# Optimization experiments

Hardware: AMD Instinct MI355X
Metric: run time of the kernel (lower is better)

The kernel has to match this reference:

```python
import jax, jax.numpy as jnp
import numpy as np

N_USERS = 60000
N_ITEMS = 40000
N = N_USERS + N_ITEMS   # ncount
EMB = 64
NNZ = 3200000           # nnz of sparse_norm_adj (avg degree 32)
LN_EPS = 1e-5


def setup_inputs() -> dict:
    key = jax.random.key(0)
    ks = jax.random.split(key, 12)
    ego = jax.random.normal(ks[0], (N, EMB), jnp.float32) * 0.1
    rows = jax.random.randint(ks[1], (NNZ,), 0, N)
    cols = jax.random.randint(ks[2], (NNZ,), 0, N)
    # normalized adjacency values (non-trainable buffer)
    vals = jax.random.uniform(ks[3], (NNZ,), jnp.float32) * 0.01
    # xavier-uniform-ish scale for [64,64]: sqrt(2/(64+64)) = 0.125
    w_uu = jax.random.normal(ks[4], (EMB, EMB), jnp.float32) * 0.125
    filt_uu = jax.random.uniform(ks[5], (N_USERS,), jnp.float32, 0.99, 1.01)
    par_uu = jax.random.uniform(ks[6], (2,), jnp.float32, 0.0, 0.99)
    w_ii = jax.random.normal(ks[7], (EMB, EMB), jnp.float32) * 0.125
    filt_ii = jax.random.uniform(ks[8], (N_ITEMS,), jnp.float32, 0.99, 1.01)
    par_ii = jax.random.uniform(ks[9], (2,), jnp.float32, 0.0, 0.99)
    ln_gamma = jnp.ones((EMB,), jnp.float32)
    ln_beta = jnp.zeros((EMB,), jnp.float32)
    return {"ego_embeddings": ego, "rows": rows, "cols": cols, "vals": vals,
            "w_uu": w_uu, "filt_uu": filt_uu, "par_uu": par_uu,
            "w_ii": w_ii, "filt_ii": filt_ii, "par_ii": par_ii,
            "ln_gamma": ln_gamma, "ln_beta": ln_beta}


def _spmm(rows, cols, vals, x):
    # out[rows] += vals * x[cols]  <=>  sparse_adj @ x
    return jax.ops.segment_sum(vals[:, None] * x[cols], rows, num_segments=N)


def reference(ego_embeddings, rows, cols, vals, w_uu, filt_uu, par_uu,
              w_ii, filt_ii, par_ii, ln_gamma, ln_beta):
    res = ego_embeddings
    u = ego_embeddings[:N_USERS]
    it = ego_embeddings[N_USERS:]
    # HWNN layer with K1=K2=1 collapses to par0*par1 * diag(filter) @ X @ W
    user_ego = par_uu[0] * par_uu[1] * ((filt_uu[:, None] * u) @ w_uu) + u
    item_ego = par_ii[0] * par_ii[1] * ((filt_ii[:, None] * it) @ w_ii) + it
    ego = jnp.concatenate([user_ego, item_ego], axis=0)  # [N, EMB]
    # HGCNConv (act=False): adj @ (adj.T @ ego)
    h = jax.ops.segment_sum(vals[:, None] * ego[rows], cols, num_segments=N)  # adj.T @ ego
    y = _spmm(rows, cols, vals, h)                                            # adj @ h
    # LayerNorm (eps=1e-5, affine) + residual from the ORIGINAL input
    mu = jnp.mean(y, axis=-1, keepdims=True)
    var = jnp.var(y, axis=-1, keepdims=True)
    yn = (y - mu) / jnp.sqrt(var + LN_EPS) * ln_gamma + ln_beta
    out = yn + res
    return out[:N_USERS], out[N_USERS:]
```

## Files before the change

kernel.cpp:

```cpp
#include <hip/hip_runtime.h>

#define N_USERS 60000
#define N_ITEMS 40000
#define N_TOTAL 100000
#define EMB 64
#define LN_EPS 1e-5f

#define KPS 512
#define KSH 9
#define NSUP ((N_TOTAL + KPS - 1) / KPS)
#define EPB 4096
#define TR_ROWS 32
#define XPITCH 68
#define CAP 3584

__device__ __forceinline__ float bf2f(unsigned short h)
{ return __uint_as_float(((unsigned)h) << 16); }
__device__ __forceinline__ unsigned short f2bf(float f)
{
    unsigned u = __float_as_uint(f);
    return (unsigned short)((u + 0x7FFFu + ((u >> 16) & 1u)) >> 16);
}

__global__ void transform_tile(const float* __restrict__ x,
                               const float* __restrict__ w_uu,
                               const float* __restrict__ filt_uu,
                               const float* __restrict__ par_uu,
                               const float* __restrict__ w_ii,
                               const float* __restrict__ filt_ii,
                               const float* __restrict__ par_ii,
                               unsigned short* __restrict__ out)
{
    __shared__ float Wls[EMB * EMB];
    __shared__ float xs[TR_ROWS * XPITCH];
    const int tid = threadIdx.x;
    const int r0 = blockIdx.x * TR_ROWS;
    const int itm = (r0 >= N_USERS);
    const float* W  = itm ? w_ii : w_uu;
    const float* fb = itm ? filt_ii : filt_uu;
    const int foff  = itm ? N_USERS : 0;
    const float c   = itm ? par_ii[0] * par_ii[1] : par_uu[0] * par_uu[1];

    for (int i = tid; i < EMB * EMB / 4; i += 256)
        ((float4*)Wls)[i] = ((const float4*)W)[i];
    for (int i = tid; i < TR_ROWS * 16; i += 256) {
        const float4 v = ((const float4*)x)[r0 * 16 + i];
        *(float4*)&xs[(i >> 4) * XPITCH + (i & 15) * 4] = v;
    }
    __syncthreads();

    const int lane = tid & 63;
    const int wv = tid >> 6;
    const int rg = lane >> 4;
    const int j  = lane & 15;

#pragma unroll
    for (int it = 0; it < 2; ++it) {
        const int rl = wv * 8 + it * 4 + rg;
        const int row = r0 + rl;
        float4 acc = make_float4(0.f, 0.f, 0.f, 0.f);
#pragma unroll 8
        for (int k = 0; k < EMB; ++k) {
            const float xb = xs[rl * XPITCH + k];
            const float4 w4 = *(const float4*)&Wls[k * EMB + 4 * j];
            acc.x += xb * w4.x; acc.y += xb * w4.y;
            acc.z += xb * w4.z; acc.w += xb * w4.w;
        }
        const float cf = c * fb[row - foff];
        const float4 xv = *(const float4*)&xs[rl * XPITCH + 4 * j];
        ushort4 o;
        o.x = f2bf(cf * acc.x + xv.x);
        o.y = f2bf(cf * acc.y + xv.y);
        o.z = f2bf(cf * acc.z + xv.z);
        o.w = f2bf(cf * acc.w + xv.w);
        *(ushort4*)&out[(size_t)row * EMB + 4 * j] = o;
    }
}

__global__ void hist_sup(const int* __restrict__ rows,
                         const int* __restrict__ cols,
                         int* __restrict__ cnt_r,
                         int* __restrict__ cnt_c, int nnz)
{
    __shared__ int hr[NSUP], hc[NSUP];
    const int tid = threadIdx.x;
    for (int i = tid; i < NSUP; i += 256) { hr[i] = 0; hc[i] = 0; }
    __syncthreads();
    for (int e = blockIdx.x * 256 + tid; e < nnz; e += gridDim.x * 256) {
        atomicAdd(&hr[rows[e] >> KSH], 1);
        atomicAdd(&hc[cols[e] >> KSH], 1);
    }
    __syncthreads();
    for (int i = tid; i < NSUP; i += 256) {
        if (hr[i]) atomicAdd(&cnt_r[i], hr[i]);
        if (hc[i]) atomicAdd(&cnt_c[i], hc[i]);
    }
}

__global__ void scan_sup(const int* __restrict__ cnt_c, int* __restrict__ base_c,
                         int* __restrict__ cur_c,
                         const int* __restrict__ cnt_r, int* __restrict__ base_r,
                         int* __restrict__ cur_r)
{
    const int* cnt = blockIdx.x ? cnt_r : cnt_c;
    int* base = blockIdx.x ? base_r : base_c;
    int* cur  = blockIdx.x ? cur_r  : cur_c;
    __shared__ int wsum[4];
    const int lane = threadIdx.x & 63;
    const int wv = threadIdx.x >> 6;
    const int i = threadIdx.x;
    const int v = (i < NSUP) ? cnt[i] : 0;
    int incl = v;
#pragma unroll
    for (int off = 1; off < 64; off <<= 1) {
        const int t = __shfl_up(incl, off, 64);
        if (lane >= off) incl += t;
    }
    if (lane == 63) wsum[wv] = incl;
    __syncthreads();
    int woff = 0;
    for (int w = 0; w < wv; ++w) woff += wsum[w];
    const int excl = woff + incl - v;
    if (i < NSUP) { base[i] = excl; cur[i] = excl; }
    if (i == 0) base[NSUP] = wsum[0] + wsum[1] + wsum[2] + wsum[3];
}

__global__ void __launch_bounds__(256, 1)
build_l1(const int* __restrict__ key,
         const int* __restrict__ other,
         const float* __restrict__ vals,
         int* __restrict__ cursor,
         int2* __restrict__ pairs1, int nnz)
{
    __shared__ int2 stage[EPB];
    __shared__ unsigned char sg[EPB];
    __shared__ int hist[NSUP];
    __shared__ int sexcl[NSUP];
    __shared__ int gbase[NSUP];
    __shared__ int lcur[NSUP];
    __shared__ int wsum[4];

    const int tid = threadIdx.x;
    const int e0 = blockIdx.x * EPB;
    const int ecnt = min(EPB, nnz - e0);

    for (int i = tid; i < NSUP; i += 256) hist[i] = 0;
    __syncthreads();

    int myk[16], myo[16];
    float myv[16];
#pragma unroll
    for (int i = 0; i < 16; ++i) {
        const int s = tid + i * 256;
        if (s < ecnt) {
            const int e = e0 + s;
            myk[i] = key[e]; myo[i] = other[e]; myv[i] = vals[e];
            atomicAdd(&hist[myk[i] >> KSH], 1);
        } else myk[i] = -1;
    }
    __syncthreads();

    {
        const int lane = tid & 63;
        const int wv = tid >> 6;
        const int v = (tid < NSUP) ? hist[tid] : 0;
        int incl = v;
#pragma unroll
        for (int off = 1; off < 64; off <<= 1) {
            const int t = __shfl_up(incl, off, 64);
            if (lane >= off) incl += t;
        }
        if (lane == 63) wsum[wv] = incl;
        __syncthreads();
        int woff = 0;
        for (int w = 0; w < wv; ++w) woff += wsum[w];
        const int excl = woff + incl - v;
        if (tid < NSUP) {
            sexcl[tid] = excl;
            lcur[tid] = excl;
            gbase[tid] = v ? atomicAdd(&cursor[tid], v) : 0;
        }
    }
    __syncthreads();

#pragma unroll
    for (int i = 0; i < 16; ++i) {
        if (myk[i] >= 0) {
            const int g = myk[i] >> KSH;
            const int s = atomicAdd(&lcur[g], 1);
            stage[s] = make_int2(myo[i] | ((myk[i] & (KPS - 1)) << 20),
                                 __float_as_int(myv[i]));
            sg[s] = (unsigned char)g;
        }
    }
    __syncthreads();

    for (int s = tid; s < ecnt; s += 256) {
        const int g = sg[s];
        pairs1[gbase[g] + (s - sexcl[g])] = stage[s];
    }
}

template <bool LN>
__global__ void __launch_bounds__(1024, 1)
spmm_fused(const int* __restrict__ base,
           const int2* __restrict__ pairs,
           const unsigned short* __restrict__ src,
           const float* __restrict__ ego,
           const float* __restrict__ gamma,
           const float* __restrict__ beta,
           unsigned short* __restrict__ dstb,
           float* __restrict__ dstf)
{
    __shared__ int2 stage[CAP];
    __shared__ int2 sorted[CAP];
    __shared__ int cnt[KPS];
    __shared__ int kbase[KPS];
    __shared__ int kcur[KPS];

    const int tid = threadIdx.x;
    const int sup = blockIdx.x;
    const int beg = base[sup];
    const int end = base[sup + 1];
    const int g = tid >> 4;
    const int l = tid & 15;

    float4 acc[8];
#pragma unroll
    for (int i = 0; i < 8; ++i) acc[i] = make_float4(0.f, 0.f, 0.f, 0.f);

    if (tid < KPS) cnt[tid] = 0;
    __syncthreads();

    int c0 = beg;
    int csz = min(CAP, end - c0);
    for (int i = tid; i < csz; i += 1024) {
        const int2 v = pairs[c0 + i];
        stage[i] = v;
        atomicAdd(&cnt[(v.x >> 20) & (KPS - 1)], 1);
    }
    __syncthreads();

    while (csz > 0) {
        if (tid < 64) {
            int c[8]; int tsum = 0;
#pragma unroll
            for (int u = 0; u < 8; ++u) { c[u] = cnt[tid * 8 + u]; tsum += c[u]; }
            int incl = tsum;
#pragma unroll
            for (int off = 1; off < 64; off <<= 1) {
                const int t = __shfl_up(incl, off, 64);
                if (tid >= off) incl += t;
            }
            int run = incl - tsum;
#pragma unroll
            for (int u = 0; u < 8; ++u) {
                kbase[tid * 8 + u] = run;
                kcur[tid * 8 + u]  = run;
                run += c[u];
                cnt[tid * 8 + u] = 0;
            }
        }
        __syncthreads();

        for (int i = tid; i < csz; i += 1024) {
            const int2 v = stage[i];
            const int pos = atomicAdd(&kcur[(v.x >> 20) & (KPS - 1)], 1);
            sorted[pos] = v;
        }
        __syncthreads();

        const int nc0 = c0 + csz;
        const int ncsz = min(CAP, end - nc0);

#pragma unroll
        for (int rr = 0; rr < 8; ++rr) {
            const int k = g * 8 + rr;
            int j = kbase[k];
            const int e = kcur[k];
            float4 a = acc[rr];
            for (; j + 4 <= e; j += 4) {
                const int2 p0 = sorted[j];
                const int2 p1 = sorted[j + 1];
                const int2 p2 = sorted[j + 2];
                const int2 p3 = sorted[j + 3];
                const ushort4 s0 = ((const ushort4*)(src + (size_t)(p0.x & 0x1FFFF) * EMB))[l];
                const ushort4 s1 = ((const ushort4*)(src + (size_t)(p1.x & 0x1FFFF) * EMB))[l];
                const ushort4 s2 = ((const ushort4*)(src + (size_t)(p2.x & 0x1FFFF) * EMB))[l];
                const ushort4 s3 = ((const ushort4*)(src + (size_t)(p3.x & 0x1FFFF) * EMB))[l];
                const float v0 = __int_as_float(p0.y);
                const float v1 = __int_as_float(p1.y);
                const float v2 = __int_as_float(p2.y);
                const float v3 = __int_as_float(p3.y);
                a.x += v0 * bf2f(s0.x); a.y += v0 * bf2f(s0.y);
                a.z += v0 * bf2f(s0.z); a.w += v0 * bf2f(s0.w);
                a.x += v1 * bf2f(s1.x); a.y += v1 * bf2f(s1.y);
                a.z += v1 * bf2f(s1.z); a.w += v1 * bf2f(s1.w);
                a.x += v2 * bf2f(s2.x); a.y += v2 * bf2f(s2.y);
                a.z += v2 * bf2f(s2.z); a.w += v2 * bf2f(s2.w);
                a.x += v3 * bf2f(s3.x); a.y += v3 * bf2f(s3.y);
                a.z += v3 * bf2f(s3.z); a.w += v3 * bf2f(s3.w);
            }
            for (; j < e; ++j) {
                const int2 p = sorted[j];
                const ushort4 s = ((const ushort4*)(src + (size_t)(p.x & 0x1FFFF) * EMB))[l];
                const float v = __int_as_float(p.y);
                a.x += v * bf2f(s.x); a.y += v * bf2f(s.y);
                a.z += v * bf2f(s.z); a.w += v * bf2f(s.w);
            }
            acc[rr] = a;
        }

        for (int i = tid; i < ncsz; i += 1024) {
            const int2 v = pairs[nc0 + i];
            stage[i] = v;
            atomicAdd(&cnt[(v.x >> 20) & (KPS - 1)], 1);
        }
        c0 = nc0; csz = ncsz;
        __syncthreads();
    }

    const int r0 = sup * KPS + g * 8;
    if (!LN) {
#pragma unroll
        for (int rr = 0; rr < 8; ++rr) {
            const int row = r0 + rr;
            if (row < N_TOTAL) {
                ushort4 o;
                o.x = f2bf(acc[rr].x); o.y = f2bf(acc[rr].y);
                o.z = f2bf(acc[rr].z); o.w = f2bf(acc[rr].w);
                ((ushort4*)dstb)[(size_t)row * 16 + l] = o;
            }
        }
    } else {
        const float4 gm = ((const float4*)gamma)[l];
        const float4 bt = ((const float4*)beta)[l];
#pragma unroll
        for (int rr = 0; rr < 8; ++rr) {
            const int row = r0 + rr;
            const float4 a = acc[rr];
            float s  = a.x + a.y + a.z + a.w;
            float s2 = a.x * a.x + a.y * a.y + a.z * a.z + a.w * a.w;
#pragma unroll
            for (int m = 1; m <= 8; m <<= 1) {
                s  += __shfl_xor(s,  m, 64);
                s2 += __shfl_xor(s2, m, 64);
            }
            const float mu  = s * (1.0f / EMB);
            const float var = s2 * (1.0f / EMB) - mu * mu;
            const float inv = rsqrtf(var + LN_EPS);
            if (row < N_TOTAL) {
                const float4 eg = ((const float4*)(ego + (size_t)row * EMB))[l];
                float4 o;
                o.x = (a.x - mu) * inv * gm.x + bt.x + eg.x;
                o.y = (a.y - mu) * inv * gm.y + bt.y + eg.y;
                o.z = (a.z - mu) * inv * gm.z + bt.z + eg.z;
                o.w = (a.w - mu) * inv * gm.w + bt.w + eg.w;
                ((float4*)(dstf + (size_t)row * EMB))[l] = o;
            }
        }
    }
}

__global__ void transform_kernel(const float* __restrict__ x,
                                 const float* __restrict__ W,
                                 const float* __restrict__ filt,
                                 const float* __restrict__ par,
                                 float* __restrict__ out, int nrows)
{
    __shared__ float Ws[EMB * EMB];
    const int tid = threadIdx.x;
    for (int i = tid; i < EMB * EMB; i += blockDim.x) Ws[i] = W[i];
    __syncthreads();
    const float c = par[0] * par[1];
    const int lane = tid & 63;
    const int wave = tid >> 6;
    const int r0 = blockIdx.x * 32;
    for (int rr = wave; rr < 32; rr += 4) {
        const int r = r0 + rr;
        if (r >= nrows) break;
        const float xv = x[(size_t)r * EMB + lane];
        float acc = 0.f;
#pragma unroll
        for (int k = 0; k < EMB; ++k) {
            const float xk = __shfl(xv, k, 64);
            acc += xk * Ws[k * EMB + lane];
        }
        out[(size_t)r * EMB + lane] = c * filt[r] * acc + xv;
    }
}

__global__ void spmm_scatter(const int* __restrict__ src_idx,
                             const int* __restrict__ dst_idx,
                             const float* __restrict__ vals,
                             const float* __restrict__ src,
                             float* __restrict__ dst, int nnz)
{
    const long long t = (long long)blockIdx.x * blockDim.x + threadIdx.x;
    const int e = (int)(t >> 4);
    const int l = (int)(t & 15);
    if (e >= nnz) return;
    const int s = src_idx[e];
    const int d = dst_idx[e];
    const float v = vals[e];
    const float4 xv = ((const float4*)(src + (size_t)s * EMB))[l];
    float* dp = dst + (size_t)d * EMB + l * 4;
    atomicAdd(dp + 0, v * xv.x);
    atomicAdd(dp + 1, v * xv.y);
    atomicAdd(dp + 2, v * xv.z);
    atomicAdd(dp + 3, v * xv.w);
}

__global__ void ln_residual(const float* y,
                            const float* __restrict__ ego,
                            const float* __restrict__ gamma,
                            const float* __restrict__ beta,
                            float* out, int nrows)
{
    const int lane = threadIdx.x & 63;
    const int wave = threadIdx.x >> 6;
    const int r = blockIdx.x * 4 + wave;
    if (r >= nrows) return;
    const float v = y[(size_t)r * EMB + lane];
    float s = v, s2 = v * v;
#pragma unroll
    for (int off = 32; off > 0; off >>= 1) {
        s  += __shfl_down(s,  off, 64);
        s2 += __shfl_down(s2, off, 64);
    }
    s  = __shfl(s,  0, 64);
    s2 = __shfl(s2, 0, 64);
    const float mu  = s * (1.0f / EMB);
    const float var = s2 * (1.0f / EMB) - mu * mu;
    const float inv = rsqrtf(var + LN_EPS);
    out[(size_t)r * EMB + lane] =
        (v - mu) * inv * gamma[lane] + beta[lane] + ego[(size_t)r * EMB + lane];
}

extern "C" void kernel_launch(void* const* d_in, const int* in_sizes, int n_in,
                              void* d_out, int out_size, void* d_ws, size_t ws_size,
                              hipStream_t stream)
{
    const float* ego     = (const float*)d_in[0];
    const int*   rows    = (const int*)  d_in[1];
    const int*   cols    = (const int*)  d_in[2];
    const float* vals    = (const float*)d_in[3];
    const float* w_uu    = (const float*)d_in[4];
    const float* filt_uu = (const float*)d_in[5];
    const float* par_uu  = (const float*)d_in[6];
    const float* w_ii    = (const float*)d_in[7];
    const float* filt_ii = (const float*)d_in[8];
    const float* par_ii  = (const float*)d_in[9];
    const float* gamma   = (const float*)d_in[10];
    const float* beta    = (const float*)d_in[11];
    float* out = (float*)d_out;
    const int nnz = in_sizes[1];

    const size_t emb_elems = (size_t)N_TOTAL * EMB;
    const size_t emb_bytes = emb_elems * sizeof(float);
    const size_t bf_bytes  = emb_elems * sizeof(unsigned short);

    const size_t need = 2 * bf_bytes + (size_t)nnz * sizeof(int2)
                        + (size_t)(6 * (NSUP + 1)) * sizeof(int);

    if (ws_size >= need) {
        unsigned short* ego2b = (unsigned short*)d_ws;
        unsigned short* hb    = ego2b + emb_elems;
        int2* pairs1 = (int2*)(hb + emb_elems);
        int*  cnt_c  = (int*)(pairs1 + nnz);
        int*  cnt_r  = cnt_c + NSUP;
        int*  base_c = cnt_r + NSUP;
        int*  cur_c  = base_c + (NSUP + 1);
        int*  base_r = cur_c + NSUP;
        int*  cur_r  = base_r + (NSUP + 1);

        hipMemsetAsync(cnt_c, 0, 2 * NSUP * sizeof(int), stream);

        hist_sup<<<512, 256, 0, stream>>>(rows, cols, cnt_r, cnt_c, nnz);
        scan_sup<<<2, 256, 0, stream>>>(cnt_c, base_c, cur_c,
                                        cnt_r, base_r, cur_r);

        transform_tile<<<N_TOTAL / TR_ROWS, 256, 0, stream>>>(
            ego, w_uu, filt_uu, par_uu, w_ii, filt_ii, par_ii, ego2b);

        const int l1b = (nnz + EPB - 1) / EPB;

        build_l1<<<l1b, 256, 0, stream>>>(cols, rows, vals, cur_c, pairs1, nnz);
        spmm_fused<false><<<NSUP, 1024, 0, stream>>>(
            base_c, pairs1, ego2b, nullptr, nullptr, nullptr, hb, nullptr);

        build_l1<<<l1b, 256, 0, stream>>>(rows, cols, vals, cur_r, pairs1, nnz);
        spmm_fused<true><<<NSUP, 1024, 0, stream>>>(
            base_r, pairs1, hb, ego, gamma, beta, nullptr, out);
    } else {
        float* ego2 = (float*)d_ws;
        float* h    = ego2 + emb_elems;
        hipMemsetAsync(h,   0, emb_bytes, stream);
        hipMemsetAsync(out, 0, emb_bytes, stream);

        transform_kernel<<<(N_USERS + 31) / 32, 256, 0, stream>>>(
            ego, w_uu, filt_uu, par_uu, ego2, N_USERS);
        transform_kernel<<<(N_ITEMS + 31) / 32, 256, 0, stream>>>(
            ego + (size_t)N_USERS * EMB, w_ii, filt_ii, par_ii,
            ego2 + (size_t)N_USERS * EMB, N_ITEMS);

        const long long thr = (long long)nnz * 16;
        const int sblocks = (int)((thr + 255) / 256);
        spmm_scatter<<<sblocks, 256, 0, stream>>>(rows, cols, vals, ego2, h, nnz);
        spmm_scatter<<<sblocks, 256, 0, stream>>>(cols, rows, vals, h, out, nnz);

        const int rb = (N_TOTAL + 3) / 4;
        ln_residual<<<rb, 256, 0, stream>>>(out, ego, gamma, beta, out, N_TOTAL);
    }
}
```

Baseline: 430.2 us.

## Shrink SpMM super-rows to 128 and prefetch next chunk into registers

Reduces rows per block from 512 to 128, with 512-thread blocks and a smaller staging capacity, so about 782 blocks run instead of 196. This spreads work across more CUs and raises occupancy. The next chunk of pairs is now loaded into registers before the accumulation loop, so its global-load latency overlaps compute. The scan and bucketing kernels are adapted to handle 782 buckets, using 4 bins per thread and 16-bit bucket ids. The cost is more per-block overhead, more atomics on the cursors, and smaller sort chunks.

```diff
diff --git a/kernel.cpp b/kernel.cpp
--- a/kernel.cpp
+++ b/kernel.cpp
@@ -6,13 +6,14 @@
 #define EMB 64
 #define LN_EPS 1e-5f
 
-#define KPS 512
-#define KSH 9
+#define KPS 128
+#define KSH 7
 #define NSUP ((N_TOTAL + KPS - 1) / KPS)
 #define EPB 4096
 #define TR_ROWS 32
 #define XPITCH 68
-#define CAP 3584
+#define CAP 2048
+#define SPT 512
 
 __device__ __forceinline__ float bf2f(unsigned short h)
 { return __uint_as_float(((unsigned)h) << 16); }
@@ -105,10 +106,10 @@
     const int* cnt = blockIdx.x ? cnt_r : cnt_c;
     int* base = blockIdx.x ? base_r : base_c;
     int* cur  = blockIdx.x ? cur_r  : cur_c;
-    __shared__ int wsum[4];
-    const int lane = threadIdx.x & 63;
-    const int wv = threadIdx.x >> 6;
+    __shared__ int wsum[16];
     const int i = threadIdx.x;
+    const int lane = i & 63;
+    const int wv = i >> 6;
     const int v = (i < NSUP) ? cnt[i] : 0;
     int incl = v;
 #pragma unroll
@@ -118,11 +119,15 @@
     }
     if (lane == 63) wsum[wv] = incl;
     __syncthreads();
-    int woff = 0;
-    for (int w = 0; w < wv; ++w) woff += wsum[w];
-    const int excl = woff + incl - v;
+    if (i == 0) {
+        int run = 0;
+#pragma unroll
+        for (int w = 0; w < 16; ++w) { const int t = wsum[w]; wsum[w] = run; run += t; }
+        base[NSUP] = run;
+    }
+    __syncthreads();
+    const int excl = wsum[wv] + incl - v;
     if (i < NSUP) { base[i] = excl; cur[i] = excl; }
-    if (i == 0) base[NSUP] = wsum[0] + wsum[1] + wsum[2] + wsum[3];
 }
 
 __global__ void __launch_bounds__(256, 1)
@@ -133,9 +138,8 @@
          int2* __restrict__ pairs1, int nnz)
 {
     __shared__ int2 stage[EPB];
-    __shared__ unsigned char sg[EPB];
+    __shared__ unsigned short sg[EPB];
     __shared__ int hist[NSUP];
-    __shared__ int sexcl[NSUP];
     __shared__ int gbase[NSUP];
     __shared__ int lcur[NSUP];
     __shared__ int wsum[4];
@@ -163,8 +167,14 @@
     {
         const int lane = tid & 63;
         const int wv = tid >> 6;
-        const int v = (tid < NSUP) ? hist[tid] : 0;
-        int incl = v;
+        int loc[4]; int tsum = 0;
+#pragma unroll
+        for (int u = 0; u < 4; ++u) {
+            const int idx = tid * 4 + u;
+            const int v = (idx < NSUP) ? hist[idx] : 0;
+            loc[u] = tsum; tsum += v;
+        }
+        int incl = tsum;
 #pragma unroll
         for (int off = 1; off < 64; off <<= 1) {
             const int t = __shfl_up(incl, off, 64);
@@ -174,11 +184,17 @@
         __syncthreads();
         int woff = 0;
         for (int w = 0; w < wv; ++w) woff += wsum[w];
-        const int excl = woff + incl - v;
-        if (tid < NSUP) {
-            sexcl[tid] = excl;
-            lcur[tid] = excl;
-            gbase[tid] = v ? atomicAdd(&cursor[tid], v) : 0;
+        const int texcl = woff + incl - tsum;
+#pragma unroll
+        for (int u = 0; u < 4; ++u) {
+            const int idx = tid * 4 + u;
+            if (idx < NSUP) {
+                const int v = hist[idx];
+                const int e = texcl + loc[u];
+                lcur[idx] = e;
+                gbase[idx] = v ? atomicAdd(&cursor[idx], v) : 0;
+                hist[idx] = e;
+            }
         }
     }
     __syncthreads();
@@ -190,19 +206,19 @@
             const int s = atomicAdd(&lcur[g], 1);
             stage[s] = make_int2(myo[i] | ((myk[i] & (KPS - 1)) << 20),
                                  __float_as_int(myv[i]));
-            sg[s] = (unsigned char)g;
+            sg[s] = (unsigned short)g;
         }
     }
     __syncthreads();
 
     for (int s = tid; s < ecnt; s += 256) {
         const int g = sg[s];
-        pairs1[gbase[g] + (s - sexcl[g])] = stage[s];
+        pairs1[gbase[g] + (s - hist[g])] = stage[s];
     }
 }
 
 template <bool LN>
-__global__ void __launch_bounds__(1024, 1)
+__global__ void __launch_bounds__(SPT, 8)
 spmm_fused(const int* __restrict__ base,
            const int2* __restrict__ pairs,
            const unsigned short* __restrict__ src,
@@ -225,16 +241,16 @@
     const int g = tid >> 4;
     const int l = tid & 15;
 
-    float4 acc[8];
-#pragma unroll
-    for (int i = 0; i < 8; ++i) acc[i] = make_float4(0.f, 0.f, 0.f, 0.f);
+    float4 acc[4];
+#pragma unroll
+    for (int i = 0; i < 4; ++i) acc[i] = make_float4(0.f, 0.f, 0.f, 0.f);
 
     if (tid < KPS) cnt[tid] = 0;
     __syncthreads();
 
     int c0 = beg;
     int csz = min(CAP, end - c0);
-    for (int i = tid; i < csz; i += 1024) {
+    for (int i = tid; i < csz; i += SPT) {
         const int2 v = pairs[c0 + i];
         stage[i] = v;
         atomicAdd(&cnt[(v.x >> 20) & (KPS - 1)], 1);
@@ -243,27 +259,23 @@
 
     while (csz > 0) {
         if (tid < 64) {
-            int c[8]; int tsum = 0;
-#pragma unroll
-            for (int u = 0; u < 8; ++u) { c[u] = cnt[tid * 8 + u]; tsum += c[u]; }
+            const int ca = cnt[tid * 2];
+            const int cb = cnt[tid * 2 + 1];
+            const int tsum = ca + cb;
             int incl = tsum;
 #pragma unroll
             for (int off = 1; off < 64; off <<= 1) {
                 const int t = __shfl_up(incl, off, 64);
                 if (tid >= off) incl += t;
             }
-            int run = incl - tsum;
-#pragma unroll
-            for (int u = 0; u < 8; ++u) {
-                kbase[tid * 8 + u] = run;
-                kcur[tid * 8 + u]  = run;
-                run += c[u];
-                cnt[tid * 8 + u] = 0;
-            }
+            const int run = incl - tsum;
+            kbase[tid * 2] = run;       kcur[tid * 2] = run;
+            kbase[tid * 2 + 1] = run + ca; kcur[tid * 2 + 1] = run + ca;
+            cnt[tid * 2] = 0; cnt[tid * 2 + 1] = 0;
         }
         __syncthreads();
 
-        for (int i = tid; i < csz; i += 1024) {
+        for (int i = tid; i < csz; i += SPT) {
             const int2 v = stage[i];
             const int pos = atomicAdd(&kcur[(v.x >> 20) & (KPS - 1)], 1);
             sorted[pos] = v;
@@ -273,9 +285,13 @@
         const int nc0 = c0 + csz;
         const int ncsz = min(CAP, end - nc0);
 
-#pragma unroll
-        for (int rr = 0; rr < 8; ++rr) {
-            const int k = g * 8 + rr;
+        int2 pre[CAP / SPT];
+        int npre = 0;
+        for (int i = tid; i < ncsz; i += SPT) pre[npre++] = pairs[nc0 + i];
+
+#pragma unroll
+        for (int rr = 0; rr < 4; ++rr) {
+            const int k = g * 4 + rr;
             int j = kbase[k];
             const int e = kcur[k];
             float4 a = acc[rr];
@@ -311,19 +327,22 @@
             acc[rr] = a;
         }
 
-        for (int i = tid; i < ncsz; i += 1024) {
-            const int2 v = pairs[nc0 + i];
-            stage[i] = v;
-            atomicAdd(&cnt[(v.x >> 20) & (KPS - 1)], 1);
+#pragma unroll
+        for (int u = 0; u < CAP / SPT; ++u) {
+            if (u < npre) {
+                const int2 v = pre[u];
+                stage[tid + u * SPT] = v;
+                atomicAdd(&cnt[(v.x >> 20) & (KPS - 1)], 1);
+            }
         }
         c0 = nc0; csz = ncsz;
         __syncthreads();
     }
 
-    const int r0 = sup * KPS + g * 8;
+    const int r0 = sup * KPS + g * 4;
     if (!LN) {
 #pragma unroll
-        for (int rr = 0; rr < 8; ++rr) {
+        for (int rr = 0; rr < 4; ++rr) {
             const int row = r0 + rr;
             if (row < N_TOTAL) {
                 ushort4 o;
@@ -336,7 +355,7 @@
         const float4 gm = ((const float4*)gamma)[l];
         const float4 bt = ((const float4*)beta)[l];
 #pragma unroll
-        for (int rr = 0; rr < 8; ++rr) {
+        for (int rr = 0; rr < 4; ++rr) {
             const int row = r0 + rr;
             const float4 a = acc[rr];
             float s  = a.x + a.y + a.z + a.w;
@@ -477,8 +496,8 @@
         hipMemsetAsync(cnt_c, 0, 2 * NSUP * sizeof(int), stream);
 
         hist_sup<<<512, 256, 0, stream>>>(rows, cols, cnt_r, cnt_c, nnz);
-        scan_sup<<<2, 256, 0, stream>>>(cnt_c, base_c, cur_c,
-                                        cnt_r, base_r, cur_r);
+        scan_sup<<<2, 1024, 0, stream>>>(cnt_c, base_c, cur_c,
+                                         cnt_r, base_r, cur_r);
 
         transform_tile<<<N_TOTAL / TR_ROWS, 256, 0, stream>>>(
             ego, w_uu, filt_uu, par_uu, w_ii, filt_ii, par_ii, ego2b);
@@ -486,11 +505,11 @@
         const int l1b = (nnz + EPB - 1) / EPB;
 
         build_l1<<<l1b, 256, 0, stream>>>(cols, rows, vals, cur_c, pairs1, nnz);
-        spmm_fused<false><<<NSUP, 1024, 0, stream>>>(
+        spmm_fused<false><<<NSUP, SPT, 0, stream>>>(
             base_c, pairs1, ego2b, nullptr, nullptr, nullptr, hb, nullptr);
 
         build_l1<<<l1b, 256, 0, stream>>>(rows, cols, vals, cur_r, pairs1, nnz);
-        spmm_fused<true><<<NSUP, 1024, 0, stream>>>(
+        spmm_fused<true><<<NSUP, SPT, 0, stream>>>(
             base_r, pairs1, hb, ego, gamma, beta, nullptr, out);
     } else {
         float* ego2 = (float*)d_ws;
```

Measured after the change: 506.4 us. 1.18x slower.
